# Kernel optimization log

Hardware: AMD Instinct MI355X
Metric: run time of the kernel (lower is better)

Reference implementation:

```python
import jax, jax.numpy as jnp
import numpy as np

BATCH, SEQ, NFEAT, HID = 128, 2048, 64, 256


def setup_inputs() -> dict:
    key = jax.random.key(0)
    ks = jax.random.split(key, 9)
    k = 1.0 / np.sqrt(HID)  # PyTorch LSTM/Linear init range
    u = lambda kk, shp: jax.random.uniform(kk, shp, jnp.float32, -k, k)
    return {
        "ts_batch": jax.random.normal(ks[0], (BATCH, SEQ, NFEAT), jnp.float32),
        "Wih_e": u(ks[1], (4 * HID, NFEAT)),
        "Whh_e": u(ks[2], (4 * HID, HID)),
        "b_e": u(ks[3], (4 * HID,)),  # b_ih + b_hh combined
        "Wih_d": u(ks[4], (4 * HID, NFEAT)),
        "Whh_d": u(ks[5], (4 * HID, HID)),
        "b_d": u(ks[6], (4 * HID,)),
        "Wout": u(ks[7], (NFEAT, HID)),
        "bout": u(ks[8], (NFEAT,)),
    }


def _lstm_cell(x, h, c, Wih, Whh, b):
    # gates: [B, 4H], PyTorch order (i, f, g, o)
    gates = x @ Wih.T + h @ Whh.T + b
    i, f, g, o = jnp.split(gates, 4, axis=-1)
    c_new = jax.nn.sigmoid(f) * c + jax.nn.sigmoid(i) * jnp.tanh(g)
    h_new = jax.nn.sigmoid(o) * jnp.tanh(c_new)
    return h_new, c_new


def reference(ts_batch, Wih_e, Whh_e, b_e, Wih_d, Whh_d, b_d, Wout, bout):
    B, T, F = ts_batch.shape
    H = Whh_e.shape[1]
    h0 = jnp.zeros((B, H), ts_batch.dtype)
    c0 = jnp.zeros((B, H), ts_batch.dtype)

    xs = jnp.swapaxes(ts_batch, 0, 1)  # [T, B, F]

    def enc_step(carry, x):
        h, c = carry
        h, c = _lstm_cell(x, h, c, Wih_e, Whh_e, b_e)
        return (h, c), None

    enc_hc, _ = jax.lax.scan(enc_step, (h0, c0), xs)

    # Decoder (training branch): for i = T-1 .. 0:
    #   output[:, i] = Linear(h)  (before update)
    #   h, c = LSTMCell(ts_batch[:, i], h, c)
    def dec_step(carry, x):
        h, c = carry
        out = h @ Wout.T + bout  # [B, F]
        h, c = _lstm_cell(x, h, c, Wih_d, Whh_d, b_d)
        return (h, c), out

    _, outs_rev = jax.lax.scan(dec_step, enc_hc, xs[::-1])
    return jnp.swapaxes(outs_rev[::-1], 0, 1)  # [B, T, F]
```

## Files before the change

kernel.cpp:

```cpp
#include <hip/hip_runtime.h>

#define TT 2048
#define FF 64
#define HH 256
#define ZSTR 344

typedef short short8 __attribute__((ext_vector_type(8)));
typedef float f32x4 __attribute__((ext_vector_type(4)));
typedef unsigned long long u64t;
typedef unsigned u32t;

#define WS_HB_B 1343488

__device__ inline unsigned short f2b(float f) {
  unsigned int u = __builtin_bit_cast(unsigned int, f);
  u += 0x7fffu + ((u >> 16) & 1u);
  return (unsigned short)(u >> 16);
}

__global__ void prep_kernel(const float* __restrict__ Wih_e, const float* __restrict__ Whh_e,
                            const float* __restrict__ Wih_d, const float* __restrict__ Whh_d,
                            const float* __restrict__ Wout, unsigned short* __restrict__ ws) {
  int idx = blockIdx.x * blockDim.x + threadIdx.x;
  if (idx >= 83968) return;
  const float* src; unsigned short* dst; int q, kdim;
  if (idx < 32768)      { q = idx;         src = Whh_e; dst = ws + 0      + q * 8; kdim = HH; }
  else if (idx < 40960) { q = idx - 32768; src = Wih_e; dst = ws + 262144 + q * 8; kdim = FF; }
  else if (idx < 73728) { q = idx - 40960; src = Whh_d; dst = ws + 327680 + q * 8; kdim = HH; }
  else if (idx < 81920) { q = idx - 73728; src = Wih_d; dst = ws + 589824 + q * 8; kdim = FF; }
  else                  { q = idx - 81920; src = Wout;  dst = ws + 655360 + q * 8; kdim = HH; }
  int ksPerTile = (kdim == HH) ? 8 : 2;
  int per = ksPerTile * 64;
  int tile = q / per, rem = q % per;
  int ks = rem / 64, l = rem % 64;
  int col = tile * 16 + (l & 15);
  int k0 = ks * 32 + (l >> 4) * 8;
#pragma unroll
  for (int e = 0; e < 8; e++) dst[e] = f2b(src[col * kdim + k0 + e]);
}

__global__ void init_hb(u64t* __restrict__ hb) {
  int i = blockIdx.x * blockDim.x + threadIdx.x;
  if (i < 32768) hb[i] = 0ull;
}

__global__ __launch_bounds__(512, 2) void lstm_kernel(
    const float* __restrict__ xg, const float* __restrict__ b_e,
    const float* __restrict__ b_d, const float* __restrict__ bout,
    const unsigned short* __restrict__ wsu, float* __restrict__ out,
    u64t* __restrict__ hb) {
  extern __shared__ unsigned short smem[];
  unsigned short* zbb = smem;
  unsigned short* wout_lds = smem + 11008;
  unsigned short* wih_lds = smem + 19200;

  const int tid = threadIdx.x;
  const int l = tid & 63, w = tid >> 6;
  const int ln = l & 15, lk = l >> 4;
  const int bb = blockIdx.x >> 1, gg = blockIdx.x & 1;
  const int b0 = bb * 16;
  const int KO = 4 * gg, KP = 4 * (1 - gg);

  {
    const short8* WoutP = (const short8*)(wsu + 655360);
    short8* wl = (short8*)wout_lds;
    wl[tid] = WoutP[gg * 1024 + tid];
    wl[tid + 512] = WoutP[gg * 1024 + tid + 512];
  }
  const float bo0 = bout[32 * gg + ln], bo1 = bout[32 * gg + 16 + ln];

  const int U = 128 * gg + 16 * w + ln;

  int cidx0, crow0, cU0, cidx1, crow1, cU1;
  {
    int m = tid, pu = m >> 3, rp = m & 7;
    cU0 = 128 * (1 - gg) + pu; cidx0 = (bb * 256 + cU0) * 8 + rp; crow0 = 2 * rp;
    m = tid + 512; pu = m >> 3; rp = m & 7;
    cU1 = 128 * (1 - gg) + pu; cidx1 = (bb * 256 + cU1) * 8 + rp; crow1 = 2 * rp;
  }
  const int p0 = (bb * 256 + U) * 8 + 2 * lk;

  float creg[4] = {0.f, 0.f, 0.f, 0.f};

  const int xrow = tid >> 5, xf = (tid & 31) * 2;
  const float* xrp = xg + (size_t)(b0 + xrow) * TT * FF + xf;
  float2 xv = *(const float2*)xrp;

#pragma unroll
  for (int i = 0; i < 4; i++) {
    int q = i * 512 + tid;
    *(u32t*)&zbb[(q >> 7) * ZSTR + (q & 127) * 2] = 0u;
  }
  *(u32t*)&zbb[xrow * ZSTR + HH + xf] = (u32t)f2b(xv.x) | ((u32t)f2b(xv.y) << 16);
  xv = *(const float2*)(xrp + FF);

  for (int ph = 0; ph < 2; ++ph) {
    const short8* WhhP = (const short8*)(wsu + (ph ? 327680 : 0));
    const short8* WihP = (const short8*)(wsu + (ph ? 589824 : 262144));
    const float* bias = ph ? b_d : b_e;

    {
      short8* wl = (short8*)wih_lds;
#pragma unroll
      for (int k = 0; k < 8; k++) {
        int i = tid + 512 * k;
        int li = i & 63, jj = (i >> 6) & 1, sub = (i >> 7) & 7, g = i >> 10;
        wl[i] = WihP[((g * 16 + 8 * gg + sub) * 2 + jj) * 64 + li];
      }
    }

    short8 rOwn[4][4], rPeer[4][4];
#pragma unroll
    for (int g = 0; g < 4; g++) {
      const int c = g * 16 + 8 * gg + w;
#pragma unroll
      for (int j = 0; j < 4; j++) {
        rOwn[g][j]  = WhhP[(c * 8 + KO + j) * 64 + l];
        rPeer[g][j] = WhhP[(c * 8 + KP + j) * 64 + l];
      }
    }

    float bact[4];
#pragma unroll
    for (int g = 0; g < 4; g++) bact[g] = bias[g * 256 + U];

    __syncthreads();

#pragma unroll 1
    for (int ti = 0; ti < TT; ++ti) {
      const int it = ph * TT + ti;
      const int t = ph ? (TT - 1 - ti) : ti;
      unsigned short* zc = zbb + (it & 1) * (16 * ZSTR);
      unsigned short* zn = zbb + ((it & 1) ^ 1) * (16 * ZSTR);

      short8 aOwn[4], aX[2];
#pragma unroll
      for (int j = 0; j < 4; j++) aOwn[j] = *(const short8*)&zc[ln * ZSTR + (KO + j) * 32 + lk * 8];
#pragma unroll
      for (int j = 0; j < 2; j++) aX[j] = *(const short8*)&zc[ln * ZSTR + (8 + j) * 32 + lk * 8];

      f32x4 acc[4];
#pragma unroll
      for (int g = 0; g < 4; g++) acc[g] = f32x4{0.f, 0.f, 0.f, 0.f};

#pragma unroll
      for (int j = 0; j < 4; j++)
#pragma unroll
        for (int g = 0; g < 4; g++)
          acc[g] = __builtin_amdgcn_mfma_f32_16x16x32_bf16(aOwn[j], rOwn[g][j], acc[g], 0, 0, 0);
#pragma unroll
      for (int j = 0; j < 2; j++)
#pragma unroll
        for (int g = 0; g < 4; g++) {
          short8 bf = ((const short8*)wih_lds)[((g * 8 + w) * 2 + j) * 64 + l];
          acc[g] = __builtin_amdgcn_mfma_f32_16x16x32_bf16(aX[j], bf, acc[g], 0, 0, 0);
        }

      if (it) {
        const u64t* base = hb + (size_t)(it & 1) * 16384;
        u64t v0 = 0, v1 = 0;
        bool d0 = false, d1 = false;
        do {
          if (!d0) { v0 = __hip_atomic_load(base + cidx0, __ATOMIC_RELAXED, __HIP_MEMORY_SCOPE_AGENT);
                     d0 = ((u32t)v0 == (u32t)it); }
          if (!d1) { v1 = __hip_atomic_load(base + cidx1, __ATOMIC_RELAXED, __HIP_MEMORY_SCOPE_AGENT);
                     d1 = ((u32t)v1 == (u32t)it); }
        } while (!(d0 && d1));
        zc[crow0 * ZSTR + cU0] = (unsigned short)(v0 >> 32);
        zc[(crow0 + 1) * ZSTR + cU0] = (unsigned short)(v0 >> 48);
        zc[crow1 * ZSTR + cU1] = (unsigned short)(v1 >> 32);
        zc[(crow1 + 1) * ZSTR + cU1] = (unsigned short)(v1 >> 48);
      }
      __syncthreads();

      short8 aPeer[4];
#pragma unroll
      for (int j = 0; j < 4; j++) aPeer[j] = *(const short8*)&zc[ln * ZSTR + (KP + j) * 32 + lk * 8];
#pragma unroll
      for (int j = 0; j < 4; j++)
#pragma unroll
        for (int g = 0; g < 4; g++)
          acc[g] = __builtin_amdgcn_mfma_f32_16x16x32_bf16(aPeer[j], rPeer[g][j], acc[g], 0, 0, 0);

      unsigned short hu[4];
#pragma unroll
      for (int r = 0; r < 4; r++) {
        float gi = acc[0][r] + bact[0];
        float gf = acc[1][r] + bact[1];
        float gG = acc[2][r] + bact[2];
        float go = acc[3][r] + bact[3];
        float si = 1.f / (1.f + __expf(-gi));
        float sf = 1.f / (1.f + __expf(-gf));
        float tg = 1.f - 2.f / (__expf(2.f * gG) + 1.f);
        float so = 1.f / (1.f + __expf(-go));
        float cn = sf * creg[r] + si * tg;
        creg[r] = cn;
        float hn = so * (1.f - 2.f / (__expf(2.f * cn) + 1.f));
        hu[r] = f2b(hn);
      }
      const u32t h01 = (u32t)hu[0] | ((u32t)hu[1] << 16);
      const u32t h23 = (u32t)hu[2] | ((u32t)hu[3] << 16);

      {
        u64t* bp = hb + (size_t)((it + 1) & 1) * 16384;
        const u64t tag = (u64t)(u32t)(it + 1);
        __hip_atomic_store(bp + p0,     tag | ((u64t)h01 << 32), __ATOMIC_RELAXED, __HIP_MEMORY_SCOPE_AGENT);
        __hip_atomic_store(bp + p0 + 1, tag | ((u64t)h23 << 32), __ATOMIC_RELAXED, __HIP_MEMORY_SCOPE_AGENT);
      }

      zn[(4 * lk + 0) * ZSTR + U] = hu[0];
      zn[(4 * lk + 1) * ZSTR + U] = hu[1];
      zn[(4 * lk + 2) * ZSTR + U] = hu[2];
      zn[(4 * lk + 3) * ZSTR + U] = hu[3];

      if (ph == 1 && w == (ti & 7)) {
        const short8* wl = (const short8*)wout_lds;
        f32x4 oa0 = {0.f, 0.f, 0.f, 0.f}, oa1 = {0.f, 0.f, 0.f, 0.f};
#pragma unroll
        for (int j = 0; j < 4; j++) {
          oa0 = __builtin_amdgcn_mfma_f32_16x16x32_bf16(aOwn[j], wl[(KO + j) * 64 + l], oa0, 0, 0, 0);
          oa1 = __builtin_amdgcn_mfma_f32_16x16x32_bf16(aOwn[j], wl[(8 + KO + j) * 64 + l], oa1, 0, 0, 0);
          oa0 = __builtin_amdgcn_mfma_f32_16x16x32_bf16(aPeer[j], wl[(KP + j) * 64 + l], oa0, 0, 0, 0);
          oa1 = __builtin_amdgcn_mfma_f32_16x16x32_bf16(aPeer[j], wl[(8 + KP + j) * 64 + l], oa1, 0, 0, 0);
        }
#pragma unroll
        for (int r = 0; r < 4; r++) {
          size_t o = ((size_t)(b0 + 4 * lk + r) * TT + t) * FF + 32 * gg;
          out[o + ln] = oa0[r] + bo0;
          out[o + 16 + ln] = oa1[r] + bo1;
        }
      }

      *(u32t*)&zn[xrow * ZSTR + HH + xf] = (u32t)f2b(xv.x) | ((u32t)f2b(xv.y) << 16);
      {
        int it2 = it + 2; if (it2 >= 2 * TT) it2 = 0;
        int t2 = (it2 < TT) ? it2 : (2 * TT - 1 - it2);
        xv = *(const float2*)(xrp + (size_t)t2 * FF);
      }
      __syncthreads();
    }
    __syncthreads();
  }
}

extern "C" void kernel_launch(void* const* d_in, const int* in_sizes, int n_in,
                              void* d_out, int out_size, void* d_ws, size_t ws_size,
                              hipStream_t stream) {
  const float* ts    = (const float*)d_in[0];
  const float* Wih_e = (const float*)d_in[1];
  const float* Whh_e = (const float*)d_in[2];
  const float* b_e   = (const float*)d_in[3];
  const float* Wih_d = (const float*)d_in[4];
  const float* Whh_d = (const float*)d_in[5];
  const float* b_d   = (const float*)d_in[6];
  const float* Wout  = (const float*)d_in[7];
  const float* bout  = (const float*)d_in[8];
  unsigned short* ws = (unsigned short*)d_ws;
  float* out = (float*)d_out;
  u64t* hb = (u64t*)((char*)d_ws + WS_HB_B);

  const int ldsBytes = 51968 * 2;
  (void)hipFuncSetAttribute((const void*)lstm_kernel,
                            hipFuncAttributeMaxDynamicSharedMemorySize, ldsBytes);

  prep_kernel<<<328, 256, 0, stream>>>(Wih_e, Whh_e, Wih_d, Whh_d, Wout, ws);
  init_hb<<<64, 512, 0, stream>>>(hb);
  lstm_kernel<<<16, 512, ldsBytes, stream>>>(ts, b_e, b_d, bout, ws, out, hb);
}
```

Measured before the change: 11.77 ms.

## Split each batch tile across eight workgroups with LDS-resident recurrent weights

Each 16-row batch tile is now handled by eight 128-thread workgroups instead of two 512-thread ones, so each workgroup owns 32 hidden units. The recurrent weights move from registers into LDS, and the h exchange through the tagged global buffer grows from one peer to seven. The aim is to spread the per-step matmul over more CUs and cut per-step latency. In exchange, every step does more cross-workgroup polling and reads its weights from LDS.

```diff
diff --git a/kernel.cpp b/kernel.cpp
--- a/kernel.cpp
+++ b/kernel.cpp
@@ -16,6 +16,9 @@
   unsigned int u = __builtin_bit_cast(unsigned int, f);
   u += 0x7fffu + ((u >> 16) & 1u);
   return (unsigned short)(u >> 16);
+}
+__device__ inline u32t pk2(float a, float b) {
+  return (u32t)f2b(a) | ((u32t)f2b(b) << 16);
 }
 
 __global__ void prep_kernel(const float* __restrict__ Wih_e, const float* __restrict__ Whh_e,
@@ -44,86 +47,91 @@
   if (i < 32768) hb[i] = 0ull;
 }
 
-__global__ __launch_bounds__(512, 2) void lstm_kernel(
+__global__ __launch_bounds__(128, 1) void lstm_kernel(
     const float* __restrict__ xg, const float* __restrict__ b_e,
     const float* __restrict__ b_d, const float* __restrict__ bout,
     const unsigned short* __restrict__ wsu, float* __restrict__ out,
     u64t* __restrict__ hb) {
   extern __shared__ unsigned short smem[];
-  unsigned short* zbb = smem;
+  unsigned short* zbb      = smem;
   unsigned short* wout_lds = smem + 11008;
-  unsigned short* wih_lds = smem + 19200;
+  unsigned short* whh_lds  = smem + 15104;
+  unsigned short* wih_lds  = smem + 47872;
 
   const int tid = threadIdx.x;
   const int l = tid & 63, w = tid >> 6;
   const int ln = l & 15, lk = l >> 4;
-  const int bb = blockIdx.x >> 1, gg = blockIdx.x & 1;
+  const int bb = blockIdx.x >> 3, gg = blockIdx.x & 7;
   const int b0 = bb * 16;
-  const int KO = 4 * gg, KP = 4 * (1 - gg);
-
-  {
+
+  if (gg < 4) {
     const short8* WoutP = (const short8*)(wsu + 655360);
     short8* wl = (short8*)wout_lds;
-    wl[tid] = WoutP[gg * 1024 + tid];
-    wl[tid + 512] = WoutP[gg * 1024 + tid + 512];
-  }
-  const float bo0 = bout[32 * gg + ln], bo1 = bout[32 * gg + 16 + ln];
-
-  const int U = 128 * gg + 16 * w + ln;
-
-  int cidx0, crow0, cU0, cidx1, crow1, cU1;
-  {
-    int m = tid, pu = m >> 3, rp = m & 7;
-    cU0 = 128 * (1 - gg) + pu; cidx0 = (bb * 256 + cU0) * 8 + rp; crow0 = 2 * rp;
-    m = tid + 512; pu = m >> 3; rp = m & 7;
-    cU1 = 128 * (1 - gg) + pu; cidx1 = (bb * 256 + cU1) * 8 + rp; crow1 = 2 * rp;
+#pragma unroll
+    for (int k = 0; k < 4; k++) wl[tid + 128 * k] = WoutP[gg * 512 + tid + 128 * k];
+  }
+  const float bo_ = (gg < 4) ? bout[16 * gg + ln] : 0.f;
+
+  const int U = 32 * gg + 16 * w + ln;
+
+  int cidx[14], crow[14], cU[14];
+#pragma unroll
+  for (int k = 0; k < 14; k++) {
+    int m = k * 128 + tid;
+    int pu = m >> 3, rp = m & 7;
+    int Up = pu + (pu >= 32 * gg ? 32 : 0);
+    cidx[k] = (bb * 256 + Up) * 8 + rp;
+    crow[k] = 2 * rp;
+    cU[k] = Up;
   }
   const int p0 = (bb * 256 + U) * 8 + 2 * lk;
 
   float creg[4] = {0.f, 0.f, 0.f, 0.f};
 
-  const int xrow = tid >> 5, xf = (tid & 31) * 2;
-  const float* xrp = xg + (size_t)(b0 + xrow) * TT * FF + xf;
-  float2 xv = *(const float2*)xrp;
-
-#pragma unroll
-  for (int i = 0; i < 4; i++) {
-    int q = i * 512 + tid;
+  const int xrow = tid >> 3, xf0 = (tid & 7) * 8;
+  const float* xrp = xg + (size_t)(b0 + xrow) * TT * FF + xf0;
+  float4 xa = *(const float4*)xrp;
+  float4 xb = *(const float4*)(xrp + 4);
+
+#pragma unroll
+  for (int i = 0; i < 16; i++) {
+    int q = i * 128 + tid;
     *(u32t*)&zbb[(q >> 7) * ZSTR + (q & 127) * 2] = 0u;
   }
-  *(u32t*)&zbb[xrow * ZSTR + HH + xf] = (u32t)f2b(xv.x) | ((u32t)f2b(xv.y) << 16);
-  xv = *(const float2*)(xrp + FF);
+  *(u32t*)&zbb[xrow * ZSTR + HH + xf0]     = pk2(xa.x, xa.y);
+  *(u32t*)&zbb[xrow * ZSTR + HH + xf0 + 2] = pk2(xa.z, xa.w);
+  *(u32t*)&zbb[xrow * ZSTR + HH + xf0 + 4] = pk2(xb.x, xb.y);
+  *(u32t*)&zbb[xrow * ZSTR + HH + xf0 + 6] = pk2(xb.z, xb.w);
+  xa = *(const float4*)(xrp + FF);
+  xb = *(const float4*)(xrp + FF + 4);
 
   for (int ph = 0; ph < 2; ++ph) {
     const short8* WhhP = (const short8*)(wsu + (ph ? 327680 : 0));
     const short8* WihP = (const short8*)(wsu + (ph ? 589824 : 262144));
     const float* bias = ph ? b_d : b_e;
 
+    __syncthreads();
     {
-      short8* wl = (short8*)wih_lds;
+      short8* wl = (short8*)whh_lds;
+#pragma unroll
+      for (int k = 0; k < 32; k++) {
+        int i = tid + 128 * k;
+        int lane = i & 63, ks = (i >> 6) & 7, tl = i >> 9;
+        int c = (tl >> 1) * 16 + 2 * gg + (tl & 1);
+        wl[i] = WhhP[(c * 8 + ks) * 64 + lane];
+      }
+      short8* wl2 = (short8*)wih_lds;
 #pragma unroll
       for (int k = 0; k < 8; k++) {
-        int i = tid + 512 * k;
-        int li = i & 63, jj = (i >> 6) & 1, sub = (i >> 7) & 7, g = i >> 10;
-        wl[i] = WihP[((g * 16 + 8 * gg + sub) * 2 + jj) * 64 + li];
+        int i = tid + 128 * k;
+        int lane = i & 63, j = (i >> 6) & 1, tl = i >> 7;
+        int c = (tl >> 1) * 16 + 2 * gg + (tl & 1);
+        wl2[i] = WihP[(c * 2 + j) * 64 + lane];
       }
     }
-
-    short8 rOwn[4][4], rPeer[4][4];
-#pragma unroll
-    for (int g = 0; g < 4; g++) {
-      const int c = g * 16 + 8 * gg + w;
-#pragma unroll
-      for (int j = 0; j < 4; j++) {
-        rOwn[g][j]  = WhhP[(c * 8 + KO + j) * 64 + l];
-        rPeer[g][j] = WhhP[(c * 8 + KP + j) * 64 + l];
-      }
-    }
-
     float bact[4];
 #pragma unroll
     for (int g = 0; g < 4; g++) bact[g] = bias[g * 256 + U];
-
     __syncthreads();
 
 #pragma unroll 1
@@ -133,54 +141,64 @@
       unsigned short* zc = zbb + (it & 1) * (16 * ZSTR);
       unsigned short* zn = zbb + ((it & 1) ^ 1) * (16 * ZSTR);
 
-      short8 aOwn[4], aX[2];
-#pragma unroll
-      for (int j = 0; j < 4; j++) aOwn[j] = *(const short8*)&zc[ln * ZSTR + (KO + j) * 32 + lk * 8];
-#pragma unroll
-      for (int j = 0; j < 2; j++) aX[j] = *(const short8*)&zc[ln * ZSTR + (8 + j) * 32 + lk * 8];
+      const short8* WH = (const short8*)whh_lds;
+      const short8* WX = (const short8*)wih_lds;
+
+      short8 aOwn = *(const short8*)&zc[ln * ZSTR + gg * 32 + lk * 8];
+      short8 aX0  = *(const short8*)&zc[ln * ZSTR + 256 + lk * 8];
+      short8 aX1  = *(const short8*)&zc[ln * ZSTR + 288 + lk * 8];
 
       f32x4 acc[4];
 #pragma unroll
       for (int g = 0; g < 4; g++) acc[g] = f32x4{0.f, 0.f, 0.f, 0.f};
-
-#pragma unroll
-      for (int j = 0; j < 4; j++)
-#pragma unroll
-        for (int g = 0; g < 4; g++)
-          acc[g] = __builtin_amdgcn_mfma_f32_16x16x32_bf16(aOwn[j], rOwn[g][j], acc[g], 0, 0, 0);
-#pragma unroll
-      for (int j = 0; j < 2; j++)
-#pragma unroll
-        for (int g = 0; g < 4; g++) {
-          short8 bf = ((const short8*)wih_lds)[((g * 8 + w) * 2 + j) * 64 + l];
-          acc[g] = __builtin_amdgcn_mfma_f32_16x16x32_bf16(aX[j], bf, acc[g], 0, 0, 0);
-        }
+#pragma unroll
+      for (int g = 0; g < 4; g++) {
+        const int tl = g * 2 + w;
+        acc[g] = __builtin_amdgcn_mfma_f32_16x16x32_bf16(aOwn, WH[(tl * 8 + gg) * 64 + l], acc[g], 0, 0, 0);
+        acc[g] = __builtin_amdgcn_mfma_f32_16x16x32_bf16(aX0,  WX[(tl * 2 + 0) * 64 + l], acc[g], 0, 0, 0);
+        acc[g] = __builtin_amdgcn_mfma_f32_16x16x32_bf16(aX1,  WX[(tl * 2 + 1) * 64 + l], acc[g], 0, 0, 0);
+      }
 
       if (it) {
         const u64t* base = hb + (size_t)(it & 1) * 16384;
-        u64t v0 = 0, v1 = 0;
-        bool d0 = false, d1 = false;
-        do {
-          if (!d0) { v0 = __hip_atomic_load(base + cidx0, __ATOMIC_RELAXED, __HIP_MEMORY_SCOPE_AGENT);
-                     d0 = ((u32t)v0 == (u32t)it); }
-          if (!d1) { v1 = __hip_atomic_load(base + cidx1, __ATOMIC_RELAXED, __HIP_MEMORY_SCOPE_AGENT);
-                     d1 = ((u32t)v1 == (u32t)it); }
-        } while (!(d0 && d1));
-        zc[crow0 * ZSTR + cU0] = (unsigned short)(v0 >> 32);
-        zc[(crow0 + 1) * ZSTR + cU0] = (unsigned short)(v0 >> 48);
-        zc[crow1 * ZSTR + cU1] = (unsigned short)(v1 >> 32);
-        zc[(crow1 + 1) * ZSTR + cU1] = (unsigned short)(v1 >> 48);
+        u64t v[14];
+        bool d[14];
+#pragma unroll
+        for (int k = 0; k < 14; k++) { v[k] = 0; d[k] = false; }
+        for (;;) {
+          bool all = true;
+#pragma unroll
+          for (int k = 0; k < 14; k++) {
+            if (!d[k]) {
+              u64t x = __hip_atomic_load(base + cidx[k], __ATOMIC_RELAXED, __HIP_MEMORY_SCOPE_AGENT);
+              if ((u32t)x == (u32t)it) { v[k] = x; d[k] = true; } else all = false;
+            }
+          }
+          if (all) break;
+        }
+#pragma unroll
+        for (int k = 0; k < 14; k++) {
+          zc[crow[k] * ZSTR + cU[k]]       = (unsigned short)(v[k] >> 32);
+          zc[(crow[k] + 1) * ZSTR + cU[k]] = (unsigned short)(v[k] >> 48);
+        }
       }
       __syncthreads();
 
-      short8 aPeer[4];
-#pragma unroll
-      for (int j = 0; j < 4; j++) aPeer[j] = *(const short8*)&zc[ln * ZSTR + (KP + j) * 32 + lk * 8];
-#pragma unroll
-      for (int j = 0; j < 4; j++)
-#pragma unroll
-        for (int g = 0; g < 4; g++)
-          acc[g] = __builtin_amdgcn_mfma_f32_16x16x32_bf16(aPeer[j], rPeer[g][j], acc[g], 0, 0, 0);
+      short8 aP[7];
+#pragma unroll
+      for (int pk = 0; pk < 7; pk++) {
+        int ks = pk + (pk >= gg ? 1 : 0);
+        aP[pk] = *(const short8*)&zc[ln * ZSTR + ks * 32 + lk * 8];
+      }
+#pragma unroll
+      for (int pk = 0; pk < 7; pk++) {
+        int ks = pk + (pk >= gg ? 1 : 0);
+#pragma unroll
+        for (int g = 0; g < 4; g++) {
+          const int tl = g * 2 + w;
+          acc[g] = __builtin_amdgcn_mfma_f32_16x16x32_bf16(aP[pk], WH[(tl * 8 + ks) * 64 + l], acc[g], 0, 0, 0);
+        }
+      }
 
       unsigned short hu[4];
 #pragma unroll
@@ -198,14 +216,14 @@
         float hn = so * (1.f - 2.f / (__expf(2.f * cn) + 1.f));
         hu[r] = f2b(hn);
       }
-      const u32t h01 = (u32t)hu[0] | ((u32t)hu[1] << 16);
-      const u32t h23 = (u32t)hu[2] | ((u32t)hu[3] << 16);
 
       {
         u64t* bp = hb + (size_t)((it + 1) & 1) * 16384;
         const u64t tag = (u64t)(u32t)(it + 1);
-        __hip_atomic_store(bp + p0,     tag | ((u64t)h01 << 32), __ATOMIC_RELAXED, __HIP_MEMORY_SCOPE_AGENT);
-        __hip_atomic_store(bp + p0 + 1, tag | ((u64t)h23 << 32), __ATOMIC_RELAXED, __HIP_MEMORY_SCOPE_AGENT);
+        __hip_atomic_store(bp + p0,     tag | ((u64t)((u32t)hu[0] | ((u32t)hu[1] << 16)) << 32),
+                           __ATOMIC_RELAXED, __HIP_MEMORY_SCOPE_AGENT);
+        __hip_atomic_store(bp + p0 + 1, tag | ((u64t)((u32t)hu[2] | ((u32t)hu[3] << 16)) << 32),
+                           __ATOMIC_RELAXED, __HIP_MEMORY_SCOPE_AGENT);
       }
 
       zn[(4 * lk + 0) * ZSTR + U] = hu[0];
@@ -213,33 +231,32 @@
       zn[(4 * lk + 2) * ZSTR + U] = hu[2];
       zn[(4 * lk + 3) * ZSTR + U] = hu[3];
 
-      if (ph == 1 && w == (ti & 7)) {
-        const short8* wl = (const short8*)wout_lds;
-        f32x4 oa0 = {0.f, 0.f, 0.f, 0.f}, oa1 = {0.f, 0.f, 0.f, 0.f};
-#pragma unroll
-        for (int j = 0; j < 4; j++) {
-          oa0 = __builtin_amdgcn_mfma_f32_16x16x32_bf16(aOwn[j], wl[(KO + j) * 64 + l], oa0, 0, 0, 0);
-          oa1 = __builtin_amdgcn_mfma_f32_16x16x32_bf16(aOwn[j], wl[(8 + KO + j) * 64 + l], oa1, 0, 0, 0);
-          oa0 = __builtin_amdgcn_mfma_f32_16x16x32_bf16(aPeer[j], wl[(KP + j) * 64 + l], oa0, 0, 0, 0);
-          oa1 = __builtin_amdgcn_mfma_f32_16x16x32_bf16(aPeer[j], wl[(8 + KP + j) * 64 + l], oa1, 0, 0, 0);
-        }
-#pragma unroll
-        for (int r = 0; r < 4; r++) {
-          size_t o = ((size_t)(b0 + 4 * lk + r) * TT + t) * FF + 32 * gg;
-          out[o + ln] = oa0[r] + bo0;
-          out[o + 16 + ln] = oa1[r] + bo1;
-        }
-      }
-
-      *(u32t*)&zn[xrow * ZSTR + HH + xf] = (u32t)f2b(xv.x) | ((u32t)f2b(xv.y) << 16);
+      if (ph == 1 && gg < 4 && w == (ti & 1)) {
+        const short8* WO = (const short8*)wout_lds;
+        f32x4 oa = {0.f, 0.f, 0.f, 0.f};
+        oa = __builtin_amdgcn_mfma_f32_16x16x32_bf16(aOwn, WO[gg * 64 + l], oa, 0, 0, 0);
+#pragma unroll
+        for (int pk = 0; pk < 7; pk++) {
+          int ks = pk + (pk >= gg ? 1 : 0);
+          oa = __builtin_amdgcn_mfma_f32_16x16x32_bf16(aP[pk], WO[ks * 64 + l], oa, 0, 0, 0);
+        }
+#pragma unroll
+        for (int r = 0; r < 4; r++)
+          out[((size_t)(b0 + 4 * lk + r) * TT + t) * FF + 16 * gg + ln] = oa[r] + bo_;
+      }
+
+      *(u32t*)&zn[xrow * ZSTR + HH + xf0]     = pk2(xa.x, xa.y);
+      *(u32t*)&zn[xrow * ZSTR + HH + xf0 + 2] = pk2(xa.z, xa.w);
+      *(u32t*)&zn[xrow * ZSTR + HH + xf0 + 4] = pk2(xb.x, xb.y);
+      *(u32t*)&zn[xrow * ZSTR + HH + xf0 + 6] = pk2(xb.z, xb.w);
       {
         int it2 = it + 2; if (it2 >= 2 * TT) it2 = 0;
         int t2 = (it2 < TT) ? it2 : (2 * TT - 1 - it2);
-        xv = *(const float2*)(xrp + (size_t)t2 * FF);
+        xa = *(const float4*)(xrp + (size_t)t2 * FF);
+        xb = *(const float4*)(xrp + (size_t)t2 * FF + 4);
       }
       __syncthreads();
     }
-    __syncthreads();
   }
 }
 
@@ -259,11 +276,11 @@
   float* out = (float*)d_out;
   u64t* hb = (u64t*)((char*)d_ws + WS_HB_B);
 
-  const int ldsBytes = 51968 * 2;
+  const int ldsBytes = 56064 * 2;
   (void)hipFuncSetAttribute((const void*)lstm_kernel,
                             hipFuncAttributeMaxDynamicSharedMemorySize, ldsBytes);
 
   prep_kernel<<<328, 256, 0, stream>>>(Wih_e, Whh_e, Wih_d, Whh_d, Wout, ws);
   init_hb<<<64, 512, 0, stream>>>(hb);
-  lstm_kernel<<<16, 512, ldsBytes, stream>>>(ts, b_e, b_d, bout, ws, out, hb);
-}
+  lstm_kernel<<<64, 128, ldsBytes, stream>>>(ts, b_e, b_d, bout, ws, out, hb);
+}
```

Result: slower. 31.97 ms (+171.7%).
